# Optimization experiments

Hardware: AMD Instinct MI355X
Metric: run time of the kernel (lower is better)

The kernel has to match this reference:

```python
import jax, jax.numpy as jnp
import numpy as np

NUM_HEADS = 4
KERNEL = 7


def setup_inputs() -> dict:
    key = jax.random.key(0)
    k = jax.random.split(key, 6)
    B, H, W, C = 4, 64, 64, 128
    kk = KERNEL
    x = jax.random.normal(k[0], (B, H, W, C), dtype=jnp.float32)
    w_qkv = jax.random.normal(k[1], (C, 3 * C), dtype=jnp.float32) * 0.02
    b_qkv = jnp.zeros((3 * C,), dtype=jnp.float32)
    rpb = jax.random.normal(k[2], (NUM_HEADS, 2 * kk - 1, 2 * kk - 1), dtype=jnp.float32) * 0.02
    w_proj = jax.random.normal(k[3], (C, C), dtype=jnp.float32) * 0.02
    b_proj = jnp.zeros((C,), dtype=jnp.float32)
    return {"x": x, "w_qkv": w_qkv, "b_qkv": b_qkv, "rpb": rpb,
            "w_proj": w_proj, "b_proj": b_proj}


def reference(x, w_qkv, b_qkv, rpb, w_proj, b_proj):
    B, H, W, C = x.shape
    nh, k = NUM_HEADS, KERNEL
    d = C // nh
    scale = d ** -0.5

    qkv = x @ w_qkv + b_qkv                      # [B,H,W,3C]
    q, kt, v = jnp.split(qkv, 3, axis=-1)
    q = q.reshape(B, H, W, nh, d) * scale
    kt = kt.reshape(B, H, W, nh, d)
    v = v.reshape(B, H, W, nh, d)

    # NATTEN window: centered, clamped at borders (window never shrinks)
    start_h = jnp.clip(jnp.arange(H) - k // 2, 0, H - k)
    start_w = jnp.clip(jnp.arange(W) - k // 2, 0, W - k)
    idx_h = start_h[:, None] + jnp.arange(k)     # [H,k] key rows per query row
    idx_w = start_w[:, None] + jnp.arange(k)     # [W,k]

    kn = kt[:, idx_h][:, :, :, idx_w]            # [B,H,k,W,k,nh,d]
    vn = v[:, idx_h][:, :, :, idx_w]             # [B,H,k,W,k,nh,d]

    scores = jnp.einsum('bxyhd,bxiyjhd->bxyhij', q, kn)  # [B,H,W,nh,k,k]

    # relative position bias: index = (key_pos - query_pos) + (k-1)
    bh = idx_h - jnp.arange(H)[:, None] + (k - 1)        # [H,k] in [0,2k-2]
    bw = idx_w - jnp.arange(W)[:, None] + (k - 1)        # [W,k]
    bias = rpb[:, bh[:, None, :, None], bw[None, :, None, :]]  # [nh,H,W,k,k]
    scores = scores + jnp.transpose(bias, (1, 2, 0, 3, 4))

    attn = jax.nn.softmax(scores.reshape(B, H, W, nh, k * k), axis=-1)
    attn = attn.reshape(B, H, W, nh, k, k)

    out = jnp.einsum('bxyhij,bxiyjhd->bxyhd', attn, vn)  # [B,H,W,nh,d]
    out = out.reshape(B, H, W, C) @ w_proj + b_proj
    return out
```

## Files before the change

### kernel.cpp

```cpp
#include <hip/hip_runtime.h>
#include <cstddef>

#define Hdim 64
#define Wdim 64
#define Cdim 128
#define NH 4
#define DH 32
#define KW 7

__global__ __launch_bounds__(256) void gemm_bias_k128(
    const float* __restrict__ A, const float* __restrict__ W,
    const float* __restrict__ bias, float* __restrict__ C, int N)
{
    constexpr int K = 128, BM = 128, BN = 64, BK = 64;
    __shared__ float As[BK][BM + 4];
    __shared__ float Ws[BK][BN];

    const int m0 = blockIdx.x * BM;
    const int n0 = blockIdx.y * BN;
    const int tid = threadIdx.x;
    const int tx = tid & 15;
    const int ty = tid >> 4;

    float acc[8][4] = {};

    for (int kc = 0; kc < K; kc += BK) {
#pragma unroll
        for (int it = 0; it < (BM * BK) / (256 * 4); ++it) {
            int idx = (it * 256 + tid) * 4;
            int m = idx >> 6;
            int k = idx & 63;
            const float4 a = *(const float4*)(A + (size_t)(m0 + m) * K + kc + k);
            As[k + 0][m] = a.x;
            As[k + 1][m] = a.y;
            As[k + 2][m] = a.z;
            As[k + 3][m] = a.w;
        }
#pragma unroll
        for (int it = 0; it < (BK * BN) / (256 * 4); ++it) {
            int idx = (it * 256 + tid) * 4;
            int k = idx >> 6;
            int n = idx & 63;
            *(float4*)(&Ws[k][n]) = *(const float4*)(W + (size_t)(kc + k) * N + n0 + n);
        }
        __syncthreads();

#pragma unroll 8
        for (int k = 0; k < BK; ++k) {
            const float4 b4  = *(const float4*)(&Ws[k][tx * 4]);
            const float4 alo = *(const float4*)(&As[k][ty * 8]);
            const float4 ahi = *(const float4*)(&As[k][ty * 8 + 4]);
            const float a_[8] = {alo.x, alo.y, alo.z, alo.w, ahi.x, ahi.y, ahi.z, ahi.w};
            const float b_[4] = {b4.x, b4.y, b4.z, b4.w};
#pragma unroll
            for (int i = 0; i < 8; ++i)
#pragma unroll
                for (int j = 0; j < 4; ++j)
                    acc[i][j] = fmaf(a_[i], b_[j], acc[i][j]);
        }
        __syncthreads();
    }

    const float4 bia = *(const float4*)(bias + n0 + tx * 4);
#pragma unroll
    for (int i = 0; i < 8; ++i) {
        const size_t m = (size_t)(m0 + ty * 8 + i);
        float4 r;
        r.x = acc[i][0] + bia.x;
        r.y = acc[i][1] + bia.y;
        r.z = acc[i][2] + bia.z;
        r.w = acc[i][3] + bia.w;
        *(float4*)(C + m * N + n0 + tx * 4) = r;
    }
}

#define TS 16
#define HALO (TS + KW - 1)
#define DPAD 36

__global__ __launch_bounds__(256) void local_attn_kernel(
    const float* __restrict__ qkv,
    const float* __restrict__ rpb,
    float* __restrict__ outp)
{
    __shared__ float kS[HALO * HALO * DPAD];
    __shared__ float vS[HALO * HALO * DPAD];
    __shared__ float rS[13 * 13];

    const int bh = blockIdx.x;
    const int b = bh >> 2;
    const int h = bh & 3;
    const int ty0 = blockIdx.y * TS;
    const int tx0 = blockIdx.z * TS;
    const int tid = threadIdx.x;

    const int lo_h = max(0, min(ty0 - 3, Hdim - KW));
    const int hi_h = min(max(ty0 + TS - 4, 0), Hdim - KW) + KW - 1;
    const int lo_w = max(0, min(tx0 - 3, Wdim - KW));
    const int hi_w = min(max(tx0 + TS - 4, 0), Wdim - KW) + KW - 1;
    const int ch = hi_h - lo_h + 1;
    const int cw = hi_w - lo_w + 1;
    const int npos = ch * cw;

    for (int idx = tid; idx < npos * 8; idx += 256) {
        const int pos = idx >> 3;
        const int dq = idx & 7;
        const int ry = pos / cw;
        const int rx = pos - ry * cw;
        const int gy = lo_h + ry;
        const int gx = lo_w + rx;
        const size_t base = ((size_t)((b * Hdim + gy) * Wdim + gx)) * 384 + h * DH + dq * 4;
        const float4 kk = *(const float4*)(qkv + base + 128);
        const float4 vv = *(const float4*)(qkv + base + 256);
        *(float4*)(&kS[pos * DPAD + dq * 4]) = kk;
        *(float4*)(&vS[pos * DPAD + dq * 4]) = vv;
    }
    for (int i = tid; i < 13 * 13; i += 256) rS[i] = rpb[h * 169 + i];
    __syncthreads();

    const int py = tid >> 4, px = tid & 15;
    const int y = ty0 + py, x = tx0 + px;
    const int sh = max(0, min(y - 3, Hdim - KW));
    const int sw = max(0, min(x - 3, Wdim - KW));
    const size_t pix = (size_t)((b * Hdim + y) * Wdim + x);

    const float scale = 0.17677669529663687f;
    float4 q[8];
#pragma unroll
    for (int i = 0; i < 8; ++i) {
        float4 t = *(const float4*)(qkv + pix * 384 + h * DH + i * 4);
        q[i].x = t.x * scale; q[i].y = t.y * scale;
        q[i].z = t.z * scale; q[i].w = t.w * scale;
    }

    const int bh0 = sh - y + 6;
    const int bw0 = sw - x + 6;

    float sc[49];
#pragma unroll
    for (int i = 0; i < KW; ++i) {
        const int ry = sh + i - lo_h;
#pragma unroll
        for (int j = 0; j < KW; ++j) {
            const int rx = sw + j - lo_w;
            const float* kp = &kS[(ry * cw + rx) * DPAD];
            float s0 = 0.f, s1 = 0.f, s2 = 0.f, s3 = 0.f;
#pragma unroll
            for (int d8 = 0; d8 < 8; ++d8) {
                const float4 k4 = *(const float4*)(kp + d8 * 4);
                s0 = fmaf(q[d8].x, k4.x, s0);
                s1 = fmaf(q[d8].y, k4.y, s1);
                s2 = fmaf(q[d8].z, k4.z, s2);
                s3 = fmaf(q[d8].w, k4.w, s3);
            }
            sc[i * KW + j] = (s0 + s1) + (s2 + s3) + rS[(bh0 + i) * 13 + (bw0 + j)];
        }
    }

    float mx = sc[0];
#pragma unroll
    for (int t = 1; t < 49; ++t) mx = fmaxf(mx, sc[t]);
    float l = 0.f;
#pragma unroll
    for (int t = 0; t < 49; ++t) { sc[t] = __expf(sc[t] - mx); l += sc[t]; }
    const float inv = 1.f / l;

    float4 o[8] = {};
#pragma unroll
    for (int i = 0; i < KW; ++i) {
        const int ry = sh + i - lo_h;
#pragma unroll
        for (int j = 0; j < KW; ++j) {
            const int rx = sw + j - lo_w;
            const float w = sc[i * KW + j] * inv;
            const float* vp = &vS[(ry * cw + rx) * DPAD];
#pragma unroll
            for (int d8 = 0; d8 < 8; ++d8) {
                const float4 v4 = *(const float4*)(vp + d8 * 4);
                o[d8].x = fmaf(w, v4.x, o[d8].x);
                o[d8].y = fmaf(w, v4.y, o[d8].y);
                o[d8].z = fmaf(w, v4.z, o[d8].z);
                o[d8].w = fmaf(w, v4.w, o[d8].w);
            }
        }
    }
#pragma unroll
    for (int d8 = 0; d8 < 8; ++d8)
        *(float4*)(outp + pix * Cdim + h * DH + d8 * 4) = o[d8];
}

extern "C" void kernel_launch(void* const* d_in, const int* in_sizes, int n_in,
                              void* d_out, int out_size, void* d_ws, size_t ws_size,
                              hipStream_t stream) {
    const float* x      = (const float*)d_in[0];
    const float* w_qkv  = (const float*)d_in[1];
    const float* b_qkv  = (const float*)d_in[2];
    const float* rpb    = (const float*)d_in[3];
    const float* w_proj = (const float*)d_in[4];
    const float* b_proj = (const float*)d_in[5];
    float* out = (float*)d_out;

    const int M = 4 * Hdim * Wdim;
    float* qkv  = (float*)d_ws;
    float* attn = qkv + (size_t)M * 384;

    dim3 blk(256);
    gemm_bias_k128<<<dim3(M / 128, 384 / 64), blk, 0, stream>>>(x, w_qkv, b_qkv, qkv, 384);
    local_attn_kernel<<<dim3(4 * NH, Hdim / TS, Wdim / TS), blk, 0, stream>>>(qkv, rpb, attn);
    gemm_bias_k128<<<dim3(M / 128, 128 / 64), blk, 0, stream>>>(attn, w_proj, b_proj, out, 128);
}
```

Measured before the change: 135.0 us.

## Store QKV in fp16 head-major layout and retile attention and GEMM kernels

The QKV GEMM now writes fp16 output in a per-head [sel][b][h][pixel][32] layout and folds the query scale into its epilogue. The attention kernel moves to 8x8 tiles with four threads per query, fp16 shared K/V, fdot2 dot products and shuffle reductions. Both GEMMs use smaller 64-row tiles so more blocks are launched. The goal is to cut memory traffic and shared-memory footprint and raise occupancy, at some cost in numeric precision from fp16 storage.

```diff
diff --git a/kernel.cpp b/kernel.cpp
--- a/kernel.cpp
+++ b/kernel.cpp
@@ -1,59 +1,258 @@
 #include <hip/hip_runtime.h>
 #include <cstddef>
+#include <cstdint>
 
 #define Hdim 64
 #define Wdim 64
-#define Cdim 128
 #define NH 4
 #define DH 32
 #define KW 7
 
-__global__ __launch_bounds__(256) void gemm_bias_k128(
-    const float* __restrict__ A, const float* __restrict__ W,
-    const float* __restrict__ bias, float* __restrict__ C, int N)
+typedef _Float16 v2h __attribute__((ext_vector_type(2)));
+
+#if defined(__has_builtin)
+#if __has_builtin(__builtin_amdgcn_fdot2)
+#define HAVE_FDOT2 1
+#endif
+#endif
+
+__device__ __forceinline__ float fdot2acc(v2h a, v2h b, float c) {
+#ifdef HAVE_FDOT2
+    return __builtin_amdgcn_fdot2(a, b, c, false);
+#else
+    return fmaf((float)a.x, (float)b.x, fmaf((float)a.y, (float)b.y, c));
+#endif
+}
+
+union F16x8 {
+    uint4 u;
+    v2h h[4];
+};
+
+__global__ __launch_bounds__(256) void gemm_qkv(
+    const float* __restrict__ A,
+    const float* __restrict__ W,
+    const float* __restrict__ bias,
+    _Float16* __restrict__ qkvh)
 {
-    constexpr int K = 128, BM = 128, BN = 64, BK = 64;
-    __shared__ float As[BK][BM + 4];
-    __shared__ float Ws[BK][BN];
-
-    const int m0 = blockIdx.x * BM;
-    const int n0 = blockIdx.y * BN;
+    __shared__ float As[32][68];
+    __shared__ float Ws[32][132];
+
+    const int m0 = blockIdx.x * 64;
+    const int sel = blockIdx.y;
+    const int n0 = sel * 128;
     const int tid = threadIdx.x;
     const int tx = tid & 15;
     const int ty = tid >> 4;
 
-    float acc[8][4] = {};
-
-    for (int kc = 0; kc < K; kc += BK) {
-#pragma unroll
-        for (int it = 0; it < (BM * BK) / (256 * 4); ++it) {
-            int idx = (it * 256 + tid) * 4;
-            int m = idx >> 6;
-            int k = idx & 63;
-            const float4 a = *(const float4*)(A + (size_t)(m0 + m) * K + kc + k);
-            As[k + 0][m] = a.x;
-            As[k + 1][m] = a.y;
-            As[k + 2][m] = a.z;
-            As[k + 3][m] = a.w;
-        }
-#pragma unroll
-        for (int it = 0; it < (BK * BN) / (256 * 4); ++it) {
-            int idx = (it * 256 + tid) * 4;
-            int k = idx >> 6;
-            int n = idx & 63;
-            *(float4*)(&Ws[k][n]) = *(const float4*)(W + (size_t)(kc + k) * N + n0 + n);
+    float acc[4][8] = {};
+
+    for (int kc = 0; kc < 128; kc += 32) {
+#pragma unroll
+        for (int it = 0; it < 2; ++it) {
+            int idx = it * 256 + tid;
+            int m = idx >> 3;
+            int k = (idx & 7) * 4;
+            const float4 a = *(const float4*)(A + (size_t)(m0 + m) * 128 + kc + k);
+            As[k + 0][m] = a.x; As[k + 1][m] = a.y;
+            As[k + 2][m] = a.z; As[k + 3][m] = a.w;
+        }
+#pragma unroll
+        for (int it = 0; it < 4; ++it) {
+            int idx = it * 256 + tid;
+            int k = idx >> 5;
+            int n = (idx & 31) * 4;
+            *(float4*)(&Ws[k][n]) = *(const float4*)(W + (size_t)(kc + k) * 384 + n0 + n);
         }
         __syncthreads();
 
 #pragma unroll 8
-        for (int k = 0; k < BK; ++k) {
-            const float4 b4  = *(const float4*)(&Ws[k][tx * 4]);
-            const float4 alo = *(const float4*)(&As[k][ty * 8]);
-            const float4 ahi = *(const float4*)(&As[k][ty * 8 + 4]);
-            const float a_[8] = {alo.x, alo.y, alo.z, alo.w, ahi.x, ahi.y, ahi.z, ahi.w};
+        for (int k = 0; k < 32; ++k) {
+            const float4 a4 = *(const float4*)(&As[k][ty * 4]);
+            const float4 b0 = *(const float4*)(&Ws[k][tx * 8]);
+            const float4 b1 = *(const float4*)(&Ws[k][tx * 8 + 4]);
+            const float a_[4] = {a4.x, a4.y, a4.z, a4.w};
+            const float b_[8] = {b0.x, b0.y, b0.z, b0.w, b1.x, b1.y, b1.z, b1.w};
+#pragma unroll
+            for (int i = 0; i < 4; ++i)
+#pragma unroll
+                for (int j = 0; j < 8; ++j)
+                    acc[i][j] = fmaf(a_[i], b_[j], acc[i][j]);
+        }
+        __syncthreads();
+    }
+
+    const float qscale = (sel == 0) ? 0.17677669529663687f : 1.0f;
+    const int h = tx >> 2;
+    const int d0 = (tx & 3) * 8;
+    float bv[8];
+#pragma unroll
+    for (int j = 0; j < 8; ++j) bv[j] = bias[n0 + tx * 8 + j];
+
+#pragma unroll
+    for (int i = 0; i < 4; ++i) {
+        const int m = m0 + ty * 4 + i;
+        const int b = m >> 12;
+        const int yx = m & 4095;
+        _Float16 tmp[8];
+#pragma unroll
+        for (int j = 0; j < 8; ++j)
+            tmp[j] = (_Float16)((acc[i][j] + bv[j]) * qscale);
+        _Float16* dst = qkvh + ((size_t)sel * 16 + b * 4 + h) * 131072 + (size_t)yx * 32 + d0;
+        *(uint4*)dst = *(const uint4*)tmp;
+    }
+}
+
+#define ATS 8
+#define AMAXPOS 196
+#define KST 40
+
+__global__ __launch_bounds__(256, 4) void local_attn(
+    const _Float16* __restrict__ qkvh,
+    const float* __restrict__ rpb,
+    float* __restrict__ outp)
+{
+    __shared__ _Float16 kS[AMAXPOS * KST];
+    __shared__ _Float16 vS[AMAXPOS * KST];
+    __shared__ float rS[169];
+
+    const int bh = blockIdx.x;
+    const int h = bh & 3;
+    const int ty0 = blockIdx.y * ATS;
+    const int tx0 = blockIdx.z * ATS;
+    const int tid = threadIdx.x;
+
+    const int lo_h = max(0, min(ty0 - 3, Hdim - KW));
+    const int hi_h = min(ty0 + ATS - 4, Hdim - KW) + KW - 1;
+    const int lo_w = max(0, min(tx0 - 3, Wdim - KW));
+    const int hi_w = min(tx0 + ATS - 4, Wdim - KW) + KW - 1;
+    const int ch = hi_h - lo_h + 1;
+    const int cw = hi_w - lo_w + 1;
+    const int npos = ch * cw;
+
+    const _Float16* kbase = qkvh + (size_t)(16 + bh) * 131072;
+    const _Float16* vbase = qkvh + (size_t)(32 + bh) * 131072;
+
+    for (int idx = tid; idx < npos * 4; idx += 256) {
+        const int pos = idx >> 2;
+        const int c = idx & 3;
+        const int ry = pos / cw;
+        const int rx = pos - ry * cw;
+        const size_t g = ((size_t)(lo_h + ry) * Wdim + (lo_w + rx)) * 32 + c * 8;
+        *(uint4*)(kS + pos * KST + c * 8) = *(const uint4*)(kbase + g);
+        *(uint4*)(vS + pos * KST + c * 8) = *(const uint4*)(vbase + g);
+    }
+    for (int i = tid; i < 169; i += 256) rS[i] = rpb[h * 169 + i];
+    __syncthreads();
+
+    const int p = tid >> 2;
+    const int q = tid & 3;
+    const int py = p >> 3, px = p & 7;
+    const int y = ty0 + py, x = tx0 + px;
+    const int sh = max(0, min(y - 3, Hdim - KW));
+    const int sw = max(0, min(x - 3, Wdim - KW));
+    const int rb = sh - lo_h;
+    const int cb = sw - lo_w;
+    const int bh0 = sh - y + 6;
+    const int bw0 = sw - x + 6;
+
+    F16x8 qf;
+    qf.u = *(const uint4*)(qkvh + (size_t)bh * 131072 + ((size_t)y * Wdim + x) * 32 + q * 8);
+
+    float sc[49];
+#pragma unroll
+    for (int i = 0; i < KW; ++i) {
+        const _Float16* kp = kS + ((rb + i) * cw + cb) * KST + q * 8;
+        const int bi = (bh0 + i) * 13 + bw0;
+#pragma unroll
+        for (int j = 0; j < KW; ++j) {
+            F16x8 kf;
+            kf.u = *(const uint4*)(kp + j * KST);
+            float s = fdot2acc(qf.h[0], kf.h[0],
+                      fdot2acc(qf.h[1], kf.h[1],
+                      fdot2acc(qf.h[2], kf.h[2],
+                      fdot2acc(qf.h[3], kf.h[3], 0.0f))));
+            s += __shfl_xor(s, 1);
+            s += __shfl_xor(s, 2);
+            sc[i * KW + j] = s + rS[bi + j];
+        }
+    }
+
+    float mx = sc[0];
+#pragma unroll
+    for (int t = 1; t < 49; ++t) mx = fmaxf(mx, sc[t]);
+    float l = 0.f;
+#pragma unroll
+    for (int t = 0; t < 49; ++t) { sc[t] = __expf(sc[t] - mx); l += sc[t]; }
+    const float inv = 1.f / l;
+
+    float o[8] = {};
+#pragma unroll
+    for (int i = 0; i < KW; ++i) {
+        const _Float16* vp = vS + ((rb + i) * cw + cb) * KST + q * 8;
+#pragma unroll
+        for (int j = 0; j < KW; ++j) {
+            F16x8 vf;
+            vf.u = *(const uint4*)(vp + j * KST);
+            const float w = sc[i * KW + j] * inv;
+#pragma unroll
+            for (int d = 0; d < 4; ++d) {
+                o[2 * d + 0] = fmaf(w, (float)vf.h[d].x, o[2 * d + 0]);
+                o[2 * d + 1] = fmaf(w, (float)vf.h[d].y, o[2 * d + 1]);
+            }
+        }
+    }
+
+    const size_t pix = (size_t)(bh >> 2) * 4096 + (size_t)y * Wdim + x;
+    float* dst = outp + pix * 128 + h * DH + q * 8;
+    *(float4*)(dst)     = make_float4(o[0], o[1], o[2], o[3]);
+    *(float4*)(dst + 4) = make_float4(o[4], o[5], o[6], o[7]);
+}
+
+__global__ __launch_bounds__(256) void gemm_proj(
+    const float* __restrict__ A,
+    const float* __restrict__ W,
+    const float* __restrict__ bias,
+    float* __restrict__ C)
+{
+    __shared__ float As[32][68];
+    __shared__ float Ws[32][64];
+
+    const int m0 = blockIdx.x * 64;
+    const int n0 = blockIdx.y * 64;
+    const int tid = threadIdx.x;
+    const int tx = tid & 15;
+    const int ty = tid >> 4;
+
+    float acc[4][4] = {};
+
+    for (int kc = 0; kc < 128; kc += 32) {
+#pragma unroll
+        for (int it = 0; it < 2; ++it) {
+            int idx = it * 256 + tid;
+            int m = idx >> 3;
+            int k = (idx & 7) * 4;
+            const float4 a = *(const float4*)(A + (size_t)(m0 + m) * 128 + kc + k);
+            As[k + 0][m] = a.x; As[k + 1][m] = a.y;
+            As[k + 2][m] = a.z; As[k + 3][m] = a.w;
+        }
+#pragma unroll
+        for (int it = 0; it < 2; ++it) {
+            int idx = it * 256 + tid;
+            int k = idx >> 4;
+            int n = (idx & 15) * 4;
+            *(float4*)(&Ws[k][n]) = *(const float4*)(W + (size_t)(kc + k) * 128 + n0 + n);
+        }
+        __syncthreads();
+
+#pragma unroll 8
+        for (int k = 0; k < 32; ++k) {
+            const float4 a4 = *(const float4*)(&As[k][ty * 4]);
+            const float4 b4 = *(const float4*)(&Ws[k][tx * 4]);
+            const float a_[4] = {a4.x, a4.y, a4.z, a4.w};
             const float b_[4] = {b4.x, b4.y, b4.z, b4.w};
 #pragma unroll
-            for (int i = 0; i < 8; ++i)
+            for (int i = 0; i < 4; ++i)
 #pragma unroll
                 for (int j = 0; j < 4; ++j)
                     acc[i][j] = fmaf(a_[i], b_[j], acc[i][j]);
@@ -63,130 +262,15 @@
 
     const float4 bia = *(const float4*)(bias + n0 + tx * 4);
 #pragma unroll
-    for (int i = 0; i < 8; ++i) {
-        const size_t m = (size_t)(m0 + ty * 8 + i);
+    for (int i = 0; i < 4; ++i) {
+        const size_t m = (size_t)(m0 + ty * 4 + i);
         float4 r;
         r.x = acc[i][0] + bia.x;
         r.y = acc[i][1] + bia.y;
         r.z = acc[i][2] + bia.z;
         r.w = acc[i][3] + bia.w;
-        *(float4*)(C + m * N + n0 + tx * 4) = r;
-    }
-}
-
-#define TS 16
-#define HALO (TS + KW - 1)
-#define DPAD 36
-
-__global__ __launch_bounds__(256) void local_attn_kernel(
-    const float* __restrict__ qkv,
-    const float* __restrict__ rpb,
-    float* __restrict__ outp)
-{
-    __shared__ float kS[HALO * HALO * DPAD];
-    __shared__ float vS[HALO * HALO * DPAD];
-    __shared__ float rS[13 * 13];
-
-    const int bh = blockIdx.x;
-    const int b = bh >> 2;
-    const int h = bh & 3;
-    const int ty0 = blockIdx.y * TS;
-    const int tx0 = blockIdx.z * TS;
-    const int tid = threadIdx.x;
-
-    const int lo_h = max(0, min(ty0 - 3, Hdim - KW));
-    const int hi_h = min(max(ty0 + TS - 4, 0), Hdim - KW) + KW - 1;
-    const int lo_w = max(0, min(tx0 - 3, Wdim - KW));
-    const int hi_w = min(max(tx0 + TS - 4, 0), Wdim - KW) + KW - 1;
-    const int ch = hi_h - lo_h + 1;
-    const int cw = hi_w - lo_w + 1;
-    const int npos = ch * cw;
-
-    for (int idx = tid; idx < npos * 8; idx += 256) {
-        const int pos = idx >> 3;
-        const int dq = idx & 7;
-        const int ry = pos / cw;
-        const int rx = pos - ry * cw;
-        const int gy = lo_h + ry;
-        const int gx = lo_w + rx;
-        const size_t base = ((size_t)((b * Hdim + gy) * Wdim + gx)) * 384 + h * DH + dq * 4;
-        const float4 kk = *(const float4*)(qkv + base + 128);
-        const float4 vv = *(const float4*)(qkv + base + 256);
-        *(float4*)(&kS[pos * DPAD + dq * 4]) = kk;
-        *(float4*)(&vS[pos * DPAD + dq * 4]) = vv;
-    }
-    for (int i = tid; i < 13 * 13; i += 256) rS[i] = rpb[h * 169 + i];
-    __syncthreads();
-
-    const int py = tid >> 4, px = tid & 15;
-    const int y = ty0 + py, x = tx0 + px;
-    const int sh = max(0, min(y - 3, Hdim - KW));
-    const int sw = max(0, min(x - 3, Wdim - KW));
-    const size_t pix = (size_t)((b * Hdim + y) * Wdim + x);
-
-    const float scale = 0.17677669529663687f;
-    float4 q[8];
-#pragma unroll
-    for (int i = 0; i < 8; ++i) {
-        float4 t = *(const float4*)(qkv + pix * 384 + h * DH + i * 4);
-        q[i].x = t.x * scale; q[i].y = t.y * scale;
-        q[i].z = t.z * scale; q[i].w = t.w * scale;
-    }
-
-    const int bh0 = sh - y + 6;
-    const int bw0 = sw - x + 6;
-
-    float sc[49];
-#pragma unroll
-    for (int i = 0; i < KW; ++i) {
-        const int ry = sh + i - lo_h;
-#pragma unroll
-        for (int j = 0; j < KW; ++j) {
-            const int rx = sw + j - lo_w;
-            const float* kp = &kS[(ry * cw + rx) * DPAD];
-            float s0 = 0.f, s1 = 0.f, s2 = 0.f, s3 = 0.f;
-#pragma unroll
-            for (int d8 = 0; d8 < 8; ++d8) {
-                const float4 k4 = *(const float4*)(kp + d8 * 4);
-                s0 = fmaf(q[d8].x, k4.x, s0);
-                s1 = fmaf(q[d8].y, k4.y, s1);
-                s2 = fmaf(q[d8].z, k4.z, s2);
-                s3 = fmaf(q[d8].w, k4.w, s3);
-            }
-            sc[i * KW + j] = (s0 + s1) + (s2 + s3) + rS[(bh0 + i) * 13 + (bw0 + j)];
-        }
-    }
-
-    float mx = sc[0];
-#pragma unroll
-    for (int t = 1; t < 49; ++t) mx = fmaxf(mx, sc[t]);
-    float l = 0.f;
-#pragma unroll
-    for (int t = 0; t < 49; ++t) { sc[t] = __expf(sc[t] - mx); l += sc[t]; }
-    const float inv = 1.f / l;
-
-    float4 o[8] = {};
-#pragma unroll
-    for (int i = 0; i < KW; ++i) {
-        const int ry = sh + i - lo_h;
-#pragma unroll
-        for (int j = 0; j < KW; ++j) {
-            const int rx = sw + j - lo_w;
-            const float w = sc[i * KW + j] * inv;
-            const float* vp = &vS[(ry * cw + rx) * DPAD];
-#pragma unroll
-            for (int d8 = 0; d8 < 8; ++d8) {
-                const float4 v4 = *(const float4*)(vp + d8 * 4);
-                o[d8].x = fmaf(w, v4.x, o[d8].x);
-                o[d8].y = fmaf(w, v4.y, o[d8].y);
-                o[d8].z = fmaf(w, v4.z, o[d8].z);
-                o[d8].w = fmaf(w, v4.w, o[d8].w);
-            }
-        }
-    }
-#pragma unroll
-    for (int d8 = 0; d8 < 8; ++d8)
-        *(float4*)(outp + pix * Cdim + h * DH + d8 * 4) = o[d8];
+        *(float4*)(C + m * 128 + n0 + tx * 4) = r;
+    }
 }
 
 extern "C" void kernel_launch(void* const* d_in, const int* in_sizes, int n_in,
@@ -200,12 +284,11 @@
     const float* b_proj = (const float*)d_in[5];
     float* out = (float*)d_out;
 
-    const int M = 4 * Hdim * Wdim;
-    float* qkv  = (float*)d_ws;
-    float* attn = qkv + (size_t)M * 384;
+    _Float16* qkvh = (_Float16*)d_ws;
+    float* attnb = (float*)((char*)d_ws + 3ULL * 16 * 4096 * 32 * 2);
 
     dim3 blk(256);
-    gemm_bias_k128<<<dim3(M / 128, 384 / 64), blk, 0, stream>>>(x, w_qkv, b_qkv, qkv, 384);
-    local_attn_kernel<<<dim3(4 * NH, Hdim / TS, Wdim / TS), blk, 0, stream>>>(qkv, rpb, attn);
-    gemm_bias_k128<<<dim3(M / 128, 128 / 64), blk, 0, stream>>>(attn, w_proj, b_proj, out, 128);
-}
+    gemm_qkv<<<dim3(16384 / 64, 3), blk, 0, stream>>>(x, w_qkv, b_qkv, qkvh);
+    local_attn<<<dim3(16, Hdim / ATS, Wdim / ATS), blk, 0, stream>>>(qkvh, rpb, attnb);
+    gemm_proj<<<dim3(16384 / 64, 2), blk, 0, stream>>>(attnb, w_proj, b_proj, out);
+}
```

After: 125.2 us. 1.08x faster.
